# Kernel optimization log

Hardware: AMD Instinct MI355X
Metric: run time of the kernel (lower is better)

## Reference

```python
import jax, jax.numpy as jnp
import numpy as np

NUM_HEADS = 16


def setup_inputs() -> dict:
    key = jax.random.key(0)
    ks = jax.random.split(key, 11)
    S, E, F = 4096, 2048, 8192
    s = lambda k, shape, fan_in: jax.random.normal(k, shape, jnp.float32) / np.sqrt(fan_in)
    return {
        "emb": jax.random.normal(ks[0], (S, E), jnp.float32),
        "Wq": s(ks[1], (E, E), E), "bq": jnp.zeros((E,), jnp.float32),
        "Wk": s(ks[2], (E, E), E), "bk": jnp.zeros((E,), jnp.float32),
        "Wv": s(ks[3], (E, E), E), "bv": jnp.zeros((E,), jnp.float32),
        "W1": s(ks[4], (E, F), E), "b1": jnp.zeros((F,), jnp.float32),
        "W2": s(ks[5], (F, E), F), "b2": jnp.zeros((E,), jnp.float32),
    }


def reference(emb, Wq, bq, Wk, bk, Wv, bv, W1, b1, W2, b2):
    S, E = emb.shape
    H = NUM_HEADS
    D = E // H
    # project and split heads -> [H, S, D]
    q = (emb @ Wq + bq).reshape(S, H, D).transpose(1, 0, 2)
    k = (emb @ Wk + bk).reshape(S, H, D).transpose(1, 0, 2)
    v = (emb @ Wv + bv).reshape(S, H, D).transpose(1, 0, 2)
    scale = jnp.asarray(D, emb.dtype) ** 0.5
    scores = jnp.einsum("hsd,htd->hst", q, k) / scale  # [H, S, S]
    # causal mask: additive -1e9 strictly above the diagonal (matches torch.triu(..., 1)*-1e9)
    mask = jnp.triu(jnp.full((S, S), -1e9, dtype=scores.dtype), k=1)
    probs = jax.nn.softmax(scores + mask, axis=-1)
    attn = jnp.einsum("hst,htd->hsd", probs, v)  # [H, S, D]
    attn = attn.transpose(1, 0, 2).reshape(S, E)  # concat heads -> [S, E]
    hidden = jnp.maximum(attn @ W1 + b1, 0.0)
    return hidden @ W2 + b2
```

## Files before the change

kernel.cpp:

```cpp
#include <hip/hip_runtime.h>

typedef __attribute__((ext_vector_type(8))) short bf16x8;
typedef __attribute__((ext_vector_type(4))) float f32x4;

static constexpr int S = 4096;
static constexpr int E = 2048;
static constexpr int F = 8192;
static constexpr int NH = 16;
static constexpr int DH = 128;

__device__ __forceinline__ unsigned short f2bf(float f) {
  unsigned u = __builtin_bit_cast(unsigned, f);
  u += 0x7FFFu + ((u >> 16) & 1u);
  return (unsigned short)(u >> 16);
}

__device__ __forceinline__ void async16(const unsigned short* g, unsigned short* l) {
  __builtin_amdgcn_global_load_lds(
      (const __attribute__((address_space(1))) unsigned int*)g,
      (__attribute__((address_space(3))) unsigned int*)l, 16, 0, 0);
}

#define BARRIER()                                     \
  do {                                                \
    asm volatile("s_barrier" ::: "memory");           \
    __builtin_amdgcn_sched_barrier(0);                \
  } while (0)
#define WAIT_LGKM0()                                  \
  do {                                                \
    asm volatile("s_waitcnt lgkmcnt(0)" ::: "memory");\
    __builtin_amdgcn_sched_barrier(0);                \
  } while (0)
#define WAIT_VM(n)                                    \
  do {                                                \
    __builtin_amdgcn_sched_barrier(0);                \
    asm volatile("s_waitcnt vmcnt(" #n ")" ::: "memory"); \
    __builtin_amdgcn_sched_barrier(0);                \
  } while (0)

__global__ __launch_bounds__(256) void cvt_bf16_kernel(const float* __restrict__ src,
                                                       unsigned short* __restrict__ dst) {
  int i = (blockIdx.x * 256 + threadIdx.x) * 4;
  float4 v = *(const float4*)(src + i);
  ushort4 o;
  o.x = f2bf(v.x); o.y = f2bf(v.y); o.z = f2bf(v.z); o.w = f2bf(v.w);
  *(ushort4*)(dst + i) = o;
}

__global__ __launch_bounds__(256) void transpose_cvt(const float* __restrict__ src,
                                                     unsigned short* __restrict__ dst,
                                                     const int Rr, const int Cc) {
  __shared__ float t[32][33];
  const int c0 = blockIdx.x * 32, r0 = blockIdx.y * 32;
  const int tx = threadIdx.x, ty = threadIdx.y;
#pragma unroll
  for (int i = 0; i < 4; ++i) {
    int r = ty + i * 8;
    t[r][tx] = src[(size_t)(r0 + r) * Cc + c0 + tx];
  }
  __syncthreads();
#pragma unroll
  for (int i = 0; i < 4; ++i) {
    int cr = ty + i * 8;
    dst[(size_t)(c0 + cr) * Rr + r0 + tx] = f2bf(t[tx][cr]);
  }
}

enum { EPI_QKV = 0, EPI_RELU = 1, EPI_OUT = 2 };

template <int EPI>
__global__ __launch_bounds__(512, 2) void gemm8(
    const unsigned short* __restrict__ A, const unsigned short* __restrict__ B,
    const int K, const int N,
    const float* __restrict__ b0, const float* __restrict__ b1f, const float* __restrict__ b2f,
    unsigned short* __restrict__ o0, unsigned short* __restrict__ o1,
    unsigned short* __restrict__ o2, float* __restrict__ of) {
  __shared__ unsigned short lA[2][256 * 64];
  __shared__ unsigned short lB[2][256 * 64];
  const int tid = threadIdx.x, w = tid >> 6, lane = tid & 63;
  const int lane15 = lane & 15, l4 = lane >> 4;
  const int wr = w >> 2, wc = w & 3;
  const int m0 = blockIdx.y * 256, n0 = blockIdx.x * 256;

  const int prow = tid >> 3;
  const int pcc = (tid & 7) ^ (prow & 7);
  const unsigned short* gA = A + (size_t)(m0 + prow) * K + pcc * 8;
  const unsigned short* gB = B + (size_t)(n0 + prow) * K + pcc * 8;
  const size_t rstep = (size_t)64 * K;
  const int lw = w * 512;

  const int pswz0 = l4 ^ (lane15 & 7);
  const int pswz1 = (4 + l4) ^ (lane15 & 7);
  const int arow = (wr * 128 + lane15) * 64;
  const int brow = (wc * 64 + lane15) * 64;

  f32x4 zero4 = {0.f, 0.f, 0.f, 0.f};
  f32x4 acc[8][4];
#pragma unroll
  for (int i = 0; i < 8; ++i)
#pragma unroll
    for (int j = 0; j < 4; ++j) acc[i][j] = zero4;

#pragma unroll
  for (int r = 0; r < 4; ++r) async16(gB + r * rstep, &lB[0][r * 4096 + lw]);
#pragma unroll
  for (int r = 0; r < 4; ++r) async16(gA + r * rstep, &lA[0][r * 4096 + lw]);
  WAIT_VM(0);
  BARRIER();

  const int NT = K >> 6;
  bf16x8 a0[4][2], bb[2][2];
  for (int t = 0; t < NT; ++t) {
    const unsigned short* lAb = lA[t & 1];
    const unsigned short* lBb = lB[t & 1];
    unsigned short* lAn = lA[(t & 1) ^ 1];
    unsigned short* lBn = lB[(t & 1) ^ 1];
    const size_t ko = (size_t)(t + 1) * 64;
    const bool nxt = (t + 1 < NT);

#pragma unroll
    for (int mi = 0; mi < 4; ++mi) {
      a0[mi][0] = *(const bf16x8*)&lAb[arow + mi * 1024 + pswz0 * 8];
      a0[mi][1] = *(const bf16x8*)&lAb[arow + mi * 1024 + pswz1 * 8];
    }
#pragma unroll
    for (int nj = 0; nj < 2; ++nj) {
      bb[nj][0] = *(const bf16x8*)&lBb[brow + nj * 1024 + pswz0 * 8];
      bb[nj][1] = *(const bf16x8*)&lBb[brow + nj * 1024 + pswz1 * 8];
    }
    if (nxt) {
      async16(gB + 0 * rstep + ko, &lBn[0 * 4096 + lw]);
      async16(gB + 1 * rstep + ko, &lBn[1 * 4096 + lw]);
    }
    BARRIER();
    WAIT_LGKM0();
    __builtin_amdgcn_s_setprio(1);
#pragma unroll
    for (int mi = 0; mi < 4; ++mi)
#pragma unroll
      for (int nj = 0; nj < 2; ++nj)
#pragma unroll
        for (int kk = 0; kk < 2; ++kk)
          acc[mi][nj] = __builtin_amdgcn_mfma_f32_16x16x32_bf16(a0[mi][kk], bb[nj][kk], acc[mi][nj], 0, 0, 0);
    __builtin_amdgcn_s_setprio(0);
    BARRIER();

#pragma unroll
    for (int nj = 0; nj < 2; ++nj) {
      bb[nj][0] = *(const bf16x8*)&lBb[brow + 2048 + nj * 1024 + pswz0 * 8];
      bb[nj][1] = *(const bf16x8*)&lBb[brow + 2048 + nj * 1024 + pswz1 * 8];
    }
    if (nxt) {
      async16(gB + 2 * rstep + ko, &lBn[2 * 4096 + lw]);
      async16(gB + 3 * rstep + ko, &lBn[3 * 4096 + lw]);
    }
    BARRIER();
    WAIT_LGKM0();
    __builtin_amdgcn_s_setprio(1);
#pragma unroll
    for (int mi = 0; mi < 4; ++mi)
#pragma unroll
      for (int nj = 0; nj < 2; ++nj)
#pragma unroll
        for (int kk = 0; kk < 2; ++kk)
          acc[mi][2 + nj] = __builtin_amdgcn_mfma_f32_16x16x32_bf16(a0[mi][kk], bb[nj][kk], acc[mi][2 + nj], 0, 0, 0);
    __builtin_amdgcn_s_setprio(0);
    if (nxt)
      WAIT_VM(4);
    else
      WAIT_VM(0);
    BARRIER();

#pragma unroll
    for (int mi = 0; mi < 4; ++mi) {
      a0[mi][0] = *(const bf16x8*)&lAb[arow + 4096 + mi * 1024 + pswz0 * 8];
      a0[mi][1] = *(const bf16x8*)&lAb[arow + 4096 + mi * 1024 + pswz1 * 8];
    }
#pragma unroll
    for (int nj = 0; nj < 2; ++nj) {
      bb[nj][0] = *(const bf16x8*)&lBb[brow + nj * 1024 + pswz0 * 8];
      bb[nj][1] = *(const bf16x8*)&lBb[brow + nj * 1024 + pswz1 * 8];
    }
    if (nxt) {
      async16(gA + 0 * rstep + ko, &lAn[0 * 4096 + lw]);
      async16(gA + 2 * rstep + ko, &lAn[2 * 4096 + lw]);
    }
    BARRIER();
    WAIT_LGKM0();
    __builtin_amdgcn_s_setprio(1);
#pragma unroll
    for (int mi = 0; mi < 4; ++mi)
#pragma unroll
      for (int nj = 0; nj < 2; ++nj)
#pragma unroll
        for (int kk = 0; kk < 2; ++kk)
          acc[4 + mi][nj] = __builtin_amdgcn_mfma_f32_16x16x32_bf16(a0[mi][kk], bb[nj][kk], acc[4 + mi][nj], 0, 0, 0);
    __builtin_amdgcn_s_setprio(0);
    BARRIER();

#pragma unroll
    for (int nj = 0; nj < 2; ++nj) {
      bb[nj][0] = *(const bf16x8*)&lBb[brow + 2048 + nj * 1024 + pswz0 * 8];
      bb[nj][1] = *(const bf16x8*)&lBb[brow + 2048 + nj * 1024 + pswz1 * 8];
    }
    if (nxt) {
      async16(gA + 1 * rstep + ko, &lAn[1 * 4096 + lw]);
      async16(gA + 3 * rstep + ko, &lAn[3 * 4096 + lw]);
    }
    BARRIER();
    WAIT_LGKM0();
    __builtin_amdgcn_s_setprio(1);
#pragma unroll
    for (int mi = 0; mi < 4; ++mi)
#pragma unroll
      for (int nj = 0; nj < 2; ++nj)
#pragma unroll
        for (int kk = 0; kk < 2; ++kk)
          acc[4 + mi][2 + nj] = __builtin_amdgcn_mfma_f32_16x16x32_bf16(a0[mi][kk], bb[nj][kk], acc[4 + mi][2 + nj], 0, 0, 0);
    __builtin_amdgcn_s_setprio(0);
    if (nxt)
      WAIT_VM(2);
    BARRIER();
  }

#pragma unroll
  for (int j = 0; j < 4; ++j) {
    const int n = n0 + wc * 64 + j * 16 + lane15;
    float bias;
    if (EPI == EPI_QKV)
      bias = (n < E) ? b0[n] : ((n < 2 * E) ? b1f[n - E] : b2f[n - 2 * E]);
    else
      bias = b0[n];
#pragma unroll
    for (int i = 0; i < 8; ++i) {
      const int mr = m0 + wr * 128 + i * 16 + l4 * 4;
      f32x4 v = acc[i][j];
#pragma unroll
      for (int r = 0; r < 4; ++r) {
        const float val = v[r] + bias;
        const int m = mr + r;
        if (EPI == EPI_QKV) {
          if (n < E)            o0[(size_t)m * E + n] = f2bf(val);
          else if (n < 2 * E)   o1[(size_t)m * E + (n - E)] = f2bf(val);
          else                  o2[(size_t)(n - 2 * E) * S + m] = f2bf(val);
        } else if (EPI == EPI_RELU) {
          o0[(size_t)m * N + n] = f2bf(fmaxf(val, 0.f));
        } else {
          of[(size_t)m * N + n] = val;
        }
      }
    }
  }
}

__global__ __launch_bounds__(256, 2) void flash_attn(const unsigned short* __restrict__ Qb,
                                                     const unsigned short* __restrict__ Kb,
                                                     const unsigned short* __restrict__ VTb,
                                                     unsigned short* __restrict__ attn) {
  const int x = blockIdx.x;
  const int h = blockIdx.y;
  const int qt = (h < 8) ? (31 - x) : x;
  const int qbase = qt * 128;
  const int tid = threadIdx.x, w = tid >> 6, lane = tid & 63;
  const int lane15 = lane & 15, l4 = lane >> 4;
  const int rowb = qbase + w * 32;

  __shared__ unsigned short lK[2][64 * 128];
  __shared__ unsigned short lV[2][128 * 64];
  __shared__ unsigned short lP[4][16 * 72];

  bf16x8 aq[2][4];
#pragma unroll
  for (int rg = 0; rg < 2; ++rg) {
    const unsigned short* qrow = Qb + (size_t)(rowb + rg * 16 + lane15) * E + h * DH + l4 * 8;
#pragma unroll
    for (int kk = 0; kk < 4; ++kk) aq[rg][kk] = *(const bf16x8*)(qrow + kk * 32);
  }

  f32x4 zero4 = {0.f, 0.f, 0.f, 0.f};
  f32x4 o[2][8];
  float psum[2][4];
#pragma unroll
  for (int rg = 0; rg < 2; ++rg) {
#pragma unroll
    for (int j = 0; j < 8; ++j) o[rg][j] = zero4;
#pragma unroll
    for (int r = 0; r < 4; ++r) psum[rg][r] = 0.f;
  }

  {
#pragma unroll
    for (int i = 0; i < 4; ++i) {
      int c = i * 256 + w * 64 + lane;
      int row = c >> 4, pg = (c & 15) ^ (row & 15);
      async16(Kb + (size_t)row * E + h * DH + pg * 8, &lK[0][(i * 256 + w * 64) * 8]);
    }
#pragma unroll
    for (int i = 0; i < 4; ++i) {
      int c = i * 256 + w * 64 + lane;
      int row = c >> 3, pg = (c & 7) ^ (row & 7);
      async16(VTb + (size_t)(h * DH + row) * S + pg * 8, &lV[0][(i * 256 + w * 64) * 8]);
    }
  }

  const float scale = 0.088388347648318447f;
  const int ktmax = 2 * qt + 1;

  for (int kt = 0; kt <= ktmax; ++kt) {
    __syncthreads();
    if (kt < ktmax) {
      const int kb2 = (kt + 1) * 64;
      const int nb = (kt + 1) & 1;
#pragma unroll
      for (int i = 0; i < 4; ++i) {
        int c = i * 256 + w * 64 + lane;
        int row = c >> 4, pg = (c & 15) ^ (row & 15);
        async16(Kb + (size_t)(kb2 + row) * E + h * DH + pg * 8, &lK[nb][(i * 256 + w * 64) * 8]);
      }
#pragma unroll
      for (int i = 0; i < 4; ++i) {
        int c = i * 256 + w * 64 + lane;
        int row = c >> 3, pg = (c & 7) ^ (row & 7);
        async16(VTb + (size_t)(h * DH + row) * S + kb2 + pg * 8, &lV[nb][(i * 256 + w * 64) * 8]);
      }
    }
    if (kt * 64 > rowb + 31) continue;
    const int buf = kt & 1;

    f32x4 sacc[2][4];
#pragma unroll
    for (int rg = 0; rg < 2; ++rg)
#pragma unroll
      for (int j = 0; j < 4; ++j) sacc[rg][j] = zero4;
#pragma unroll
    for (int kk = 0; kk < 4; ++kk)
#pragma unroll
      for (int j = 0; j < 4; ++j) {
        int pl = (kk * 4 + l4) ^ lane15;
        bf16x8 bk = *(const bf16x8*)&lK[buf][(j * 16 + lane15) * 128 + pl * 8];
        sacc[0][j] = __builtin_amdgcn_mfma_f32_16x16x32_bf16(aq[0][kk], bk, sacc[0][j], 0, 0, 0);
        sacc[1][j] = __builtin_amdgcn_mfma_f32_16x16x32_bf16(aq[1][kk], bk, sacc[1][j], 0, 0, 0);
      }

    const bool diag = (kt * 64 + 63 > rowb);
    bf16x8 ap[2][2];
#pragma unroll
    for (int rg = 0; rg < 2; ++rg) {
      float p[4][4];
      if (diag) {
#pragma unroll
        for (int j = 0; j < 4; ++j) {
          int col = kt * 64 + j * 16 + lane15;
#pragma unroll
          for (int r = 0; r < 4; ++r) {
            int row = rowb + rg * 16 + l4 * 4 + r;
            p[j][r] = (col <= row) ? __expf(sacc[rg][j][r] * scale) : 0.f;
          }
        }
      } else {
#pragma unroll
        for (int j = 0; j < 4; ++j)
#pragma unroll
          for (int r = 0; r < 4; ++r) p[j][r] = __expf(sacc[rg][j][r] * scale);
      }
#pragma unroll
      for (int r = 0; r < 4; ++r) psum[rg][r] += p[0][r] + p[1][r] + p[2][r] + p[3][r];

#pragma unroll
      for (int j = 0; j < 4; ++j)
#pragma unroll
        for (int r = 0; r < 4; ++r)
          lP[w][(l4 * 4 + r) * 72 + j * 16 + lane15] = f2bf(p[j][r]);

#pragma unroll
      for (int ks = 0; ks < 2; ++ks)
        ap[rg][ks] = *(const bf16x8*)&lP[w][lane15 * 72 + ks * 32 + l4 * 8];
    }

#pragma unroll
    for (int ks = 0; ks < 2; ++ks)
#pragma unroll
      for (int j = 0; j < 8; ++j) {
        int pl = (ks * 4 + l4) ^ (lane15 & 7);
        bf16x8 bv = *(const bf16x8*)&lV[buf][(j * 16 + lane15) * 64 + pl * 8];
        o[0][j] = __builtin_amdgcn_mfma_f32_16x16x32_bf16(ap[0][ks], bv, o[0][j], 0, 0, 0);
        o[1][j] = __builtin_amdgcn_mfma_f32_16x16x32_bf16(ap[1][ks], bv, o[1][j], 0, 0, 0);
      }
  }

#pragma unroll
  for (int rg = 0; rg < 2; ++rg) {
    float inv[4];
#pragma unroll
    for (int r = 0; r < 4; ++r) {
      float s = psum[rg][r];
#pragma unroll
      for (int off = 1; off < 16; off <<= 1) s += __shfl_xor(s, off, 16);
      inv[r] = 1.0f / s;
    }
#pragma unroll
    for (int j = 0; j < 8; ++j)
#pragma unroll
      for (int r = 0; r < 4; ++r)
        attn[(size_t)(rowb + rg * 16 + l4 * 4 + r) * E + h * DH + j * 16 + lane15] =
            f2bf(o[rg][j][r] * inv[r]);
  }
}

extern "C" void kernel_launch(void* const* d_in, const int* in_sizes, int n_in,
                              void* d_out, int out_size, void* d_ws, size_t ws_size,
                              hipStream_t stream) {
  (void)in_sizes; (void)n_in; (void)out_size; (void)ws_size;
  const float* emb = (const float*)d_in[0];
  const float* Wq  = (const float*)d_in[1];
  const float* bq  = (const float*)d_in[2];
  const float* Wk  = (const float*)d_in[3];
  const float* bk  = (const float*)d_in[4];
  const float* Wv  = (const float*)d_in[5];
  const float* bv  = (const float*)d_in[6];
  const float* W1  = (const float*)d_in[7];
  const float* b1  = (const float*)d_in[8];
  const float* W2  = (const float*)d_in[9];
  const float* b2  = (const float*)d_in[10];
  float* out = (float*)d_out;

  char* ws = (char*)d_ws;
  const size_t MB = 1024ull * 1024ull;
  unsigned short* embb   = (unsigned short*)(ws);
  unsigned short* attn   = embb;
  char* r1 = ws + 16 * MB;
  unsigned short* WqkvT  = (unsigned short*)(r1);
  unsigned short* Qb     = (unsigned short*)(r1 + 24 * MB);
  unsigned short* Kb     = (unsigned short*)(r1 + 40 * MB);
  unsigned short* VTb    = (unsigned short*)(r1 + 56 * MB);
  unsigned short* hidden = (unsigned short*)(r1);
  unsigned short* W1T    = (unsigned short*)(r1 + 72 * MB);
  unsigned short* W2T    = (unsigned short*)(r1 + 104 * MB);

  dim3 b256(256);
  dim3 b512(512);
  dim3 tb(32, 8);
  cvt_bf16_kernel<<<dim3((S * E) / 1024), b256, 0, stream>>>(emb, embb);
  transpose_cvt<<<dim3(E / 32, E / 32), tb, 0, stream>>>(Wq, WqkvT, E, E);
  transpose_cvt<<<dim3(E / 32, E / 32), tb, 0, stream>>>(Wk, WqkvT + (size_t)E * E, E, E);
  transpose_cvt<<<dim3(E / 32, E / 32), tb, 0, stream>>>(Wv, WqkvT + 2ull * E * E, E, E);
  transpose_cvt<<<dim3(F / 32, E / 32), tb, 0, stream>>>(W1, W1T, E, F);
  transpose_cvt<<<dim3(E / 32, F / 32), tb, 0, stream>>>(W2, W2T, F, E);

  gemm8<EPI_QKV><<<dim3(3 * E / 256, S / 256), b512, 0, stream>>>(
      embb, WqkvT, E, 3 * E, bq, bk, bv, Qb, Kb, VTb, nullptr);
  flash_attn<<<dim3(S / 128, NH), b256, 0, stream>>>(Qb, Kb, VTb, attn);
  gemm8<EPI_RELU><<<dim3(F / 256, S / 256), b512, 0, stream>>>(
      attn, W1T, E, F, b1, nullptr, nullptr, hidden, nullptr, nullptr, nullptr);
  gemm8<EPI_OUT><<<dim3(E / 256, S / 256), b512, 0, stream>>>(
      hidden, W2T, F, E, b2, nullptr, nullptr, nullptr, nullptr, nullptr, out);
}
```

Baseline: 906.2 us.

## Use smaller-tile GEMM for QKV and output, remap blocks for big GEMM

Adds a simpler 128x128 tile GEMM kernel (256 threads, K-step 32, double-buffered async LDS loads) and uses it for the QKV projection and the final output projection. The 256x256 kernel is kept only for the W1 GEMM, now with launch bounds set to one block per SM and a block-index remap that spreads neighbouring tiles across XCDs. It also drops the explicit lgkmcnt waits and sched barriers around its barriers. The smaller tiles give more blocks for the narrower GEMMs, which should help load balance. The costs are lower operand reuse, possible LDS bank conflicts from the unswizzled layout, and reliance on the compiler to insert the LDS waits that were removed.

```diff
diff --git a/kernel.cpp b/kernel.cpp
--- a/kernel.cpp
+++ b/kernel.cpp
@@ -21,22 +21,8 @@
       (__attribute__((address_space(3))) unsigned int*)l, 16, 0, 0);
 }
 
-#define BARRIER()                                     \
-  do {                                                \
-    asm volatile("s_barrier" ::: "memory");           \
-    __builtin_amdgcn_sched_barrier(0);                \
-  } while (0)
-#define WAIT_LGKM0()                                  \
-  do {                                                \
-    asm volatile("s_waitcnt lgkmcnt(0)" ::: "memory");\
-    __builtin_amdgcn_sched_barrier(0);                \
-  } while (0)
-#define WAIT_VM(n)                                    \
-  do {                                                \
-    __builtin_amdgcn_sched_barrier(0);                \
-    asm volatile("s_waitcnt vmcnt(" #n ")" ::: "memory"); \
-    __builtin_amdgcn_sched_barrier(0);                \
-  } while (0)
+#define BARRIER() asm volatile("s_barrier" ::: "memory")
+#define WAIT_VM(n) asm volatile("s_waitcnt vmcnt(" #n ")" ::: "memory")
 
 __global__ __launch_bounds__(256) void cvt_bf16_kernel(const float* __restrict__ src,
                                                        unsigned short* __restrict__ dst) {
@@ -69,18 +55,112 @@
 enum { EPI_QKV = 0, EPI_RELU = 1, EPI_OUT = 2 };
 
 template <int EPI>
-__global__ __launch_bounds__(512, 2) void gemm8(
+__global__ __launch_bounds__(256) void gemm_bt(
     const unsigned short* __restrict__ A, const unsigned short* __restrict__ B,
     const int K, const int N,
     const float* __restrict__ b0, const float* __restrict__ b1f, const float* __restrict__ b2f,
     unsigned short* __restrict__ o0, unsigned short* __restrict__ o1,
     unsigned short* __restrict__ o2, float* __restrict__ of) {
+  __shared__ unsigned short lA[2][128 * 32];
+  __shared__ unsigned short lB[2][128 * 32];
+  const int tid = threadIdx.x, w = tid >> 6, lane = tid & 63;
+  const int lane15 = lane & 15, l4 = lane >> 4;
+  const int m0 = blockIdx.y * 128, n0 = blockIdx.x * 128;
+  const int wr = w >> 1, wc = w & 1;
+
+  const int u0 = (w * 2 + 0) * 64 + lane;
+  const int u1 = (w * 2 + 1) * 64 + lane;
+  const unsigned short* gA0 = A + (size_t)(m0 + (u0 >> 2)) * K + (u0 & 3) * 8;
+  const unsigned short* gA1 = A + (size_t)(m0 + (u1 >> 2)) * K + (u1 & 3) * 8;
+  const unsigned short* gB0 = B + (size_t)(n0 + (u0 >> 2)) * K + (u0 & 3) * 8;
+  const unsigned short* gB1 = B + (size_t)(n0 + (u1 >> 2)) * K + (u1 & 3) * 8;
+  const int doff0 = (w * 2 + 0) * 512;
+  const int doff1 = (w * 2 + 1) * 512;
+
+  f32x4 zero4 = {0.f, 0.f, 0.f, 0.f};
+  f32x4 acc[4][4];
+#pragma unroll
+  for (int i = 0; i < 4; ++i)
+#pragma unroll
+    for (int j = 0; j < 4; ++j) acc[i][j] = zero4;
+
+  async16(gA0, &lA[0][doff0]);
+  async16(gA1, &lA[0][doff1]);
+  async16(gB0, &lB[0][doff0]);
+  async16(gB1, &lB[0][doff1]);
+
+  for (int ko = 0; ko < K; ko += 32) {
+    __syncthreads();
+    const int buf = (ko >> 5) & 1;
+    if (ko + 32 < K) {
+      const int nb = buf ^ 1;
+      async16(gA0 + ko + 32, &lA[nb][doff0]);
+      async16(gA1 + ko + 32, &lA[nb][doff1]);
+      async16(gB0 + ko + 32, &lB[nb][doff0]);
+      async16(gB1 + ko + 32, &lB[nb][doff1]);
+    }
+    bf16x8 av[4], bv[4];
+#pragma unroll
+    for (int i = 0; i < 4; ++i)
+      av[i] = *(const bf16x8*)&lA[buf][(wr * 64 + i * 16 + lane15) * 32 + l4 * 8];
+#pragma unroll
+    for (int j = 0; j < 4; ++j)
+      bv[j] = *(const bf16x8*)&lB[buf][(wc * 64 + j * 16 + lane15) * 32 + l4 * 8];
+#pragma unroll
+    for (int i = 0; i < 4; ++i)
+#pragma unroll
+      for (int j = 0; j < 4; ++j)
+        acc[i][j] = __builtin_amdgcn_mfma_f32_16x16x32_bf16(av[i], bv[j], acc[i][j], 0, 0, 0);
+  }
+
+#pragma unroll
+  for (int j = 0; j < 4; ++j) {
+    const int n = n0 + wc * 64 + j * 16 + lane15;
+    float bias;
+    if (EPI == EPI_QKV)
+      bias = (n < E) ? b0[n] : ((n < 2 * E) ? b1f[n - E] : b2f[n - 2 * E]);
+    else
+      bias = b0[n];
+#pragma unroll
+    for (int i = 0; i < 4; ++i) {
+      const int mr = m0 + wr * 64 + i * 16 + l4 * 4;
+      f32x4 v = acc[i][j];
+#pragma unroll
+      for (int r = 0; r < 4; ++r) {
+        const float val = v[r] + bias;
+        const int m = mr + r;
+        if (EPI == EPI_QKV) {
+          if (n < E)            o0[(size_t)m * E + n] = f2bf(val);
+          else if (n < 2 * E)   o1[(size_t)m * E + (n - E)] = f2bf(val);
+          else                  o2[(size_t)(n - 2 * E) * S + m] = f2bf(val);
+        } else if (EPI == EPI_RELU) {
+          o0[(size_t)m * N + n] = f2bf(fmaxf(val, 0.f));
+        } else {
+          of[(size_t)m * N + n] = val;
+        }
+      }
+    }
+  }
+}
+
+template <int EPI>
+__global__ __launch_bounds__(512, 1) void gemm8(
+    const unsigned short* __restrict__ A, const unsigned short* __restrict__ B,
+    const int K, const int N,
+    const float* __restrict__ b0,
+    unsigned short* __restrict__ o0, float* __restrict__ of) {
   __shared__ unsigned short lA[2][256 * 64];
   __shared__ unsigned short lB[2][256 * 64];
   const int tid = threadIdx.x, w = tid >> 6, lane = tid & 63;
   const int lane15 = lane & 15, l4 = lane >> 4;
   const int wr = w >> 2, wc = w & 3;
-  const int m0 = blockIdx.y * 256, n0 = blockIdx.x * 256;
+
+  const int gx = gridDim.x, gy = gridDim.y;
+  const int hw = blockIdx.y * gx + blockIdx.x;
+  const int chunk = (gx * gy) >> 3;
+  const int pos = (hw & 7) * chunk + (hw >> 3);
+  const int bx = pos / gy, by = pos % gy;
+  const int m0 = by * 256, n0 = bx * 256;
 
   const int prow = tid >> 3;
   const int pcc = (tid & 7) ^ (prow & 7);
@@ -133,7 +213,6 @@
       async16(gB + 1 * rstep + ko, &lBn[1 * 4096 + lw]);
     }
     BARRIER();
-    WAIT_LGKM0();
     __builtin_amdgcn_s_setprio(1);
 #pragma unroll
     for (int mi = 0; mi < 4; ++mi)
@@ -155,7 +234,6 @@
       async16(gB + 3 * rstep + ko, &lBn[3 * 4096 + lw]);
     }
     BARRIER();
-    WAIT_LGKM0();
     __builtin_amdgcn_s_setprio(1);
 #pragma unroll
     for (int mi = 0; mi < 4; ++mi)
@@ -186,7 +264,6 @@
       async16(gA + 2 * rstep + ko, &lAn[2 * 4096 + lw]);
     }
     BARRIER();
-    WAIT_LGKM0();
     __builtin_amdgcn_s_setprio(1);
 #pragma unroll
     for (int mi = 0; mi < 4; ++mi)
@@ -208,7 +285,6 @@
       async16(gA + 3 * rstep + ko, &lAn[3 * 4096 + lw]);
     }
     BARRIER();
-    WAIT_LGKM0();
     __builtin_amdgcn_s_setprio(1);
 #pragma unroll
     for (int mi = 0; mi < 4; ++mi)
@@ -226,11 +302,7 @@
 #pragma unroll
   for (int j = 0; j < 4; ++j) {
     const int n = n0 + wc * 64 + j * 16 + lane15;
-    float bias;
-    if (EPI == EPI_QKV)
-      bias = (n < E) ? b0[n] : ((n < 2 * E) ? b1f[n - E] : b2f[n - 2 * E]);
-    else
-      bias = b0[n];
+    const float bias = b0[n];
 #pragma unroll
     for (int i = 0; i < 8; ++i) {
       const int mr = m0 + wr * 128 + i * 16 + l4 * 4;
@@ -239,11 +311,7 @@
       for (int r = 0; r < 4; ++r) {
         const float val = v[r] + bias;
         const int m = mr + r;
-        if (EPI == EPI_QKV) {
-          if (n < E)            o0[(size_t)m * E + n] = f2bf(val);
-          else if (n < 2 * E)   o1[(size_t)m * E + (n - E)] = f2bf(val);
-          else                  o2[(size_t)(n - 2 * E) * S + m] = f2bf(val);
-        } else if (EPI == EPI_RELU) {
+        if (EPI == EPI_RELU) {
           o0[(size_t)m * N + n] = f2bf(fmaxf(val, 0.f));
         } else {
           of[(size_t)m * N + n] = val;
@@ -447,11 +515,11 @@
   transpose_cvt<<<dim3(F / 32, E / 32), tb, 0, stream>>>(W1, W1T, E, F);
   transpose_cvt<<<dim3(E / 32, F / 32), tb, 0, stream>>>(W2, W2T, F, E);
 
-  gemm8<EPI_QKV><<<dim3(3 * E / 256, S / 256), b512, 0, stream>>>(
+  gemm_bt<EPI_QKV><<<dim3(3 * E / 128, S / 128), b256, 0, stream>>>(
       embb, WqkvT, E, 3 * E, bq, bk, bv, Qb, Kb, VTb, nullptr);
   flash_attn<<<dim3(S / 128, NH), b256, 0, stream>>>(Qb, Kb, VTb, attn);
   gemm8<EPI_RELU><<<dim3(F / 256, S / 256), b512, 0, stream>>>(
-      attn, W1T, E, F, b1, nullptr, nullptr, hidden, nullptr, nullptr, nullptr);
-  gemm8<EPI_OUT><<<dim3(E / 256, S / 256), b512, 0, stream>>>(
+      attn, W1T, E, F, b1, hidden, nullptr);
+  gemm_bt<EPI_OUT><<<dim3(E / 128, S / 128), b256, 0, stream>>>(
       hidden, W2T, F, E, b2, nullptr, nullptr, nullptr, nullptr, nullptr, out);
 }
```

New measurement: 855.7 us. 5.6% less time.
